# Optimization experiments

Hardware: AMD Instinct MI355X
Metric: run time of the kernel (lower is better)

The kernel has to match this reference:

```python
import jax, jax.numpy as jnp
import numpy as np

EMBED = 256
NHEAD = 8
HDIM = EMBED // NHEAD
EPS = 1e-6


def setup_inputs() -> dict:
    key = jax.random.key(0)
    ks = jax.random.split(key, 10)
    B, L, E = 8, 8192, EMBED
    sc = 1.0 / np.sqrt(E)
    return {
        "q": jax.random.normal(ks[0], (B, L, E), jnp.float32),
        "k": jax.random.normal(ks[1], (B, L, E), jnp.float32),
        "v": jax.random.normal(ks[2], (B, L, E), jnp.float32),
        "Wq": jax.random.normal(ks[3], (E, E), jnp.float32) * sc,
        "bq": jax.random.normal(ks[4], (E,), jnp.float32) * 0.01,
        "Wk": jax.random.normal(ks[5], (E, E), jnp.float32) * sc,
        "bk": jax.random.normal(ks[6], (E,), jnp.float32) * 0.01,
        "Wv": jax.random.normal(ks[7], (E, E), jnp.float32) * sc,
        "bv": jax.random.normal(ks[8], (E,), jnp.float32) * 0.01,
        "Wm": jax.random.normal(ks[9], (E, E), jnp.float32) * sc,
    }


def _feature_map(x):
    # elu(x) + 1, the LoFTR linear-attention kernel feature map
    return jax.nn.elu(x) + 1.0


def reference(q, k, v, Wq, bq, Wk, bk, Wv, bv, Wm):
    B, L, E = q.shape
    # QKV projections (nn.Linear: x @ W.T + b), split into heads
    Q = (q @ Wq.T + bq).reshape(B, L, NHEAD, HDIM)
    K = (k @ Wk.T + bk).reshape(B, -1, NHEAD, HDIM)
    V = (v @ Wv.T + bv).reshape(B, -1, NHEAD, HDIM)

    Qf = _feature_map(Q)              # [B,L,H,D]
    Kf = _feature_map(K)              # [B,S,H,D]
    v_len = V.shape[1]
    Vn = V / v_len
    # KV: per-head outer-product accumulation over source positions
    KV = jnp.einsum("bshd,bshv->bhdv", Kf, Vn)       # [B,H,D,D]
    Ksum = Kf.sum(axis=1)                              # [B,H,D]
    Z = 1.0 / (jnp.einsum("blhd,bhd->blh", Qf, Ksum) + EPS)  # [B,L,H]
    msg = jnp.einsum("blhd,bhdv,blh->blhv", Qf, KV, Z) * v_len  # [B,L,H,D]
    # merge heads and output projection (bias=False)
    out = msg.reshape(B, L, NHEAD * HDIM) @ Wm.T
    return out
```

## Files before the change

kernel.cpp:

```cpp
#include <hip/hip_runtime.h>
#include <hip/hip_bf16.h>

#define SEQ   8192
#define NB    8
#define EMB   256
#define NHD   8
#define HDM   32
#define LDP   72

typedef __attribute__((ext_vector_type(8))) short short8;
typedef __attribute__((ext_vector_type(4))) float floatx4;
typedef __attribute__((ext_vector_type(16))) float floatx16;

__device__ __forceinline__ short f2b(float f) {
    __hip_bfloat16 h = __float2bfloat16(f);
    return __builtin_bit_cast(short, h);
}
__device__ __forceinline__ float b2f(short s) {
    unsigned u = (unsigned)(unsigned short)s << 16;
    return __builtin_bit_cast(float, u);
}

__device__ __forceinline__ void gload16(const void* g, void* l) {
    __builtin_amdgcn_global_load_lds(
        (const __attribute__((address_space(1))) unsigned*)g,
        (__attribute__((address_space(3))) unsigned*)l, 16, 0, 0);
}

__launch_bounds__(256)
__global__ void wconv_kernel(const float* __restrict__ Wq,
                             const float* __restrict__ Wk,
                             const float* __restrict__ Wv,
                             short* __restrict__ Wb) {
    const float* src = (blockIdx.y == 0) ? Wq : (blockIdx.y == 1) ? Wk : Wv;
    const int i = (blockIdx.x * 256 + threadIdx.x) * 8;
    float4 f0 = *(const float4*)(src + i);
    float4 f1 = *(const float4*)(src + i + 4);
    short8 o;
    o[0] = f2b(f0.x); o[1] = f2b(f0.y); o[2] = f2b(f0.z); o[3] = f2b(f0.w);
    o[4] = f2b(f1.x); o[5] = f2b(f1.y); o[6] = f2b(f1.z); o[7] = f2b(f1.w);
    *(short8*)(Wb + (size_t)blockIdx.y * 65536 + i) = o;
}

__launch_bounds__(256)
__global__ void qkv_kernel(const float* __restrict__ qin,
                           const float* __restrict__ kin,
                           const float* __restrict__ vin,
                           const short* __restrict__ Wb,
                           const float* __restrict__ bq,
                           const float* __restrict__ bk,
                           const float* __restrict__ bv,
                           short* __restrict__ Qf, short* __restrict__ Kf,
                           short* __restrict__ Vn,
                           float* __restrict__ Ksum) {
    __shared__ __align__(16) float As[128 * 64];
    __shared__ __align__(16) short Bs[128 * 64];
    __shared__ float colsum[128];

    const int tid  = threadIdx.x;
    const int tm   = blockIdx.x;
    const int tn   = blockIdx.y;
    const int mode = blockIdx.z;
    const int lane = tid & 63;
    const int wave = tid >> 6;
    const int wm   = (wave & 1) << 6;
    const int wn   = (wave >> 1) << 6;
    const int fr   = lane & 15;
    const int fq   = lane >> 4;

    const float* X    = (mode == 0) ? qin : (mode == 1) ? kin : vin;
    const float* bias = (mode == 0) ? bq  : (mode == 1) ? bk  : bv;
    short*       out  = (mode == 0) ? Qf  : (mode == 1) ? Kf  : Vn;

    if (mode == 1 && tid < 128) colsum[tid] = 0.f;

    const float* Xb = X + (size_t)(tm * 128) * EMB;
    const short* Wt = Wb + (size_t)mode * 65536 + (size_t)(tn * 128) * EMB;

    floatx4 acc[4][4];
    #pragma unroll
    for (int i = 0; i < 4; i++)
        #pragma unroll
        for (int j = 0; j < 4; j++)
            #pragma unroll
            for (int r = 0; r < 4; r++) acc[i][j][r] = 0.f;

    for (int kc = 0; kc < 4; kc++) {
        const int kb = kc * 64;
        #pragma unroll
        for (int u = 0; u < 8; u++) {
            const int c   = u * 256 + tid;
            const int row = c >> 4;
            const int q   = c & 15;
            const int col = (((q >> 1) ^ (row & 7)) << 3) + ((q & 1) << 2);
            gload16(Xb + (size_t)row * EMB + kb + col, &As[c * 4]);
        }
        #pragma unroll
        for (int u = 0; u < 4; u++) {
            const int c   = u * 256 + tid;
            const int row = c >> 3;
            const int q   = c & 7;
            const int col = ((q ^ (row & 7)) << 3);
            gload16(Wt + (size_t)row * EMB + kb + col, &Bs[c * 8]);
        }
        __syncthreads();
        #pragma unroll
        for (int kk = 0; kk < 64; kk += 32) {
            short8 a[4], b[4];
            #pragma unroll
            for (int i = 0; i < 4; i++) {
                const int row  = wm + i * 16 + fr;
                const int P    = (kk >> 3) + fq;
                const int base = row * 64 + (((P ^ (row & 7)) << 3));
                float4 x0 = *(const float4*)&As[base];
                float4 x1 = *(const float4*)&As[base + 4];
                short8 t;
                t[0] = f2b(x0.x); t[1] = f2b(x0.y); t[2] = f2b(x0.z); t[3] = f2b(x0.w);
                t[4] = f2b(x1.x); t[5] = f2b(x1.y); t[6] = f2b(x1.z); t[7] = f2b(x1.w);
                a[i] = t;
            }
            #pragma unroll
            for (int j = 0; j < 4; j++) {
                const int row = wn + j * 16 + fr;
                const int qB  = (kk >> 3) + fq;
                b[j] = *(const short8*)&Bs[row * 64 + ((qB ^ (row & 7)) << 3)];
            }
            #pragma unroll
            for (int i = 0; i < 4; i++)
                #pragma unroll
                for (int j = 0; j < 4; j++)
                    acc[i][j] = __builtin_amdgcn_mfma_f32_16x16x32_bf16(a[i], b[j], acc[i][j], 0, 0, 0);
        }
        __syncthreads();
    }

    const int row0 = tm * 128;
    float ks[4] = {0.f, 0.f, 0.f, 0.f};
    #pragma unroll
    for (int i = 0; i < 4; i++) {
        #pragma unroll
        for (int j = 0; j < 4; j++) {
            const int colg = tn * 128 + wn + j * 16 + fr;
            const float bia = bias[colg];
            #pragma unroll
            for (int rr = 0; rr < 4; rr++) {
                const int rowg = row0 + wm + i * 16 + fq * 4 + rr;
                float v = acc[i][j][rr] + bia;
                if (mode <= 1) v = (v > 0.f) ? (v + 1.f) : __expf(v);
                else           v *= (1.0f / (float)SEQ);
                out[(size_t)rowg * EMB + colg] = f2b(v);
                ks[j] += v;
            }
        }
    }
    if (mode == 1) {
        #pragma unroll
        for (int j = 0; j < 4; j++)
            atomicAdd(&colsum[wn + j * 16 + fr], ks[j]);
        __syncthreads();
        if (tid < 128) {
            const int b = (tm * 128) / SEQ;
            atomicAdd(&Ksum[b * EMB + tn * 128 + tid], colsum[tid]);
        }
    }
}

template <bool ATOMIC>
__launch_bounds__(256)
__global__ void kv_kernel(const short* __restrict__ Kf,
                          const short* __restrict__ Vn,
                          float* __restrict__ dst_base,
                          int kvsp) {
    __shared__ __align__(16) short Kt[32 * 256];
    __shared__ __align__(16) short Vt[32 * 256];

    const int tid  = threadIdx.x;
    const int sp   = blockIdx.x % kvsp;
    const int b    = blockIdx.x / kvsp;
    const int wave = tid >> 6;
    const int lane = tid & 63;
    const int h    = wave * 2 + (lane >> 5);
    const int l5   = lane & 31;
    const int d0   = (l5 >> 2) * 4;
    const int v0   = (l5 & 3) * 8;
    const int chunk = SEQ / kvsp;
    const size_t rowbase = (size_t)(b * SEQ + sp * chunk) * EMB;

    float acc[4][8];
    #pragma unroll
    for (int i = 0; i < 4; i++)
        #pragma unroll
        for (int j = 0; j < 8; j++) acc[i][j] = 0.f;

    for (int t0 = 0; t0 < chunk; t0 += 32) {
        __syncthreads();
        const short* ksrc = Kf + rowbase + (size_t)t0 * EMB;
        const short* vsrc = Vn + rowbase + (size_t)t0 * EMB;
        #pragma unroll
        for (int u = 0; u < 4; u++) {
            const int c   = tid + u * 256;
            const int row = c >> 5;
            const int col = (c & 31) * 8;
            *(short8*)&Kt[row * 256 + col] = *(const short8*)(ksrc + (size_t)row * EMB + col);
            *(short8*)&Vt[row * 256 + col] = *(const short8*)(vsrc + (size_t)row * EMB + col);
        }
        __syncthreads();
        #pragma unroll 4
        for (int s = 0; s < 32; s++) {
            short4 k4 = *(const short4*)&Kt[s * 256 + h * 32 + d0];
            short8 v8 = *(const short8*)&Vt[s * 256 + h * 32 + v0];
            float kf[4] = {b2f(k4.x), b2f(k4.y), b2f(k4.z), b2f(k4.w)};
            float vf[8];
            #pragma unroll
            for (int j = 0; j < 8; j++) vf[j] = b2f(v8[j]);
            #pragma unroll
            for (int i = 0; i < 4; i++)
                #pragma unroll
                for (int j = 0; j < 8; j++) acc[i][j] += kf[i] * vf[j];
        }
    }

    if (ATOMIC) {
        float* dst = dst_base + (size_t)((b * 8 + h) * 1024);
        #pragma unroll
        for (int i = 0; i < 4; i++)
            #pragma unroll
            for (int j = 0; j < 8; j++)
                atomicAdd(&dst[(d0 + i) * 32 + v0 + j], acc[i][j]);
    } else {
        float* dst = dst_base + (size_t)(((size_t)sp * NB + b) * 8 + h) * 1024;
        #pragma unroll
        for (int i = 0; i < 4; i++) {
            float4 lo = make_float4(acc[i][0], acc[i][1], acc[i][2], acc[i][3]);
            float4 hi = make_float4(acc[i][4], acc[i][5], acc[i][6], acc[i][7]);
            *(float4*)&dst[(d0 + i) * 32 + v0]     = lo;
            *(float4*)&dst[(d0 + i) * 32 + v0 + 4] = hi;
        }
    }
}

__launch_bounds__(256)
__global__ void kvred_kernel(const float* __restrict__ KVp,
                             float* __restrict__ KV, int kvsp) {
    const int i = blockIdx.x * 1024 + threadIdx.x * 4;
    float4 s = make_float4(0.f, 0.f, 0.f, 0.f);
    for (int p = 0; p < kvsp; p++) {
        float4 t = *(const float4*)&KVp[(size_t)p * 65536 + i];
        s.x += t.x; s.y += t.y; s.z += t.z; s.w += t.w;
    }
    *(float4*)&KV[i] = s;
}

__launch_bounds__(64)
__global__ void m_kernel(const float* __restrict__ KV,
                         const float* __restrict__ Wm,
                         short* __restrict__ Mt) {
    const int blk  = blockIdx.x;
    const int e0   = (blk & 7) * 32;
    const int h    = (blk >> 3) & 7;
    const int b    = blk >> 6;
    const int lane = threadIdx.x;
    const int l31  = lane & 31;
    const int q    = lane >> 5;

    floatx16 acc;
    #pragma unroll
    for (int i = 0; i < 16; i++) acc[i] = 0.f;

    #pragma unroll
    for (int kb = 0; kb < 32; kb += 16) {
        const float* ar = KV + (size_t)(((b * 8 + h) * 32 + l31) * 32) + kb + q * 8;
        const float* br = Wm + (size_t)(e0 + l31) * EMB + h * 32 + kb + q * 8;
        short8 a, w;
        #pragma unroll
        for (int t = 0; t < 8; t++) { a[t] = f2b(ar[t]); w[t] = f2b(br[t]); }
        acc = __builtin_amdgcn_mfma_f32_32x32x16_bf16(a, w, acc, 0, 0, 0);
    }

    short* mrow = Mt + (size_t)b * EMB * EMB + (size_t)(e0 + l31) * EMB + h * 32;
    #pragma unroll
    for (int r4 = 0; r4 < 4; r4++) {
        const int dbase = 8 * r4 + 4 * q;
        short4 s4 = make_short4(f2b(acc[r4 * 4 + 0]), f2b(acc[r4 * 4 + 1]),
                                f2b(acc[r4 * 4 + 2]), f2b(acc[r4 * 4 + 3]));
        *(short4*)(mrow + dbase) = s4;
    }
}

__launch_bounds__(256)
__global__ void out_kernel(const short* __restrict__ Qf,
                           const float* __restrict__ Ksum,
                           const short* __restrict__ Mt,
                           float* __restrict__ Out) {
    __shared__ __align__(16) short As[128 * LDP];
    __shared__ __align__(16) short Bs[128 * LDP];
    __shared__ float zs[128][NHD];
    __shared__ float ksl[EMB];

    const int tid  = threadIdx.x;
    const int tm   = blockIdx.x;
    const int tn   = blockIdx.y;
    const int b    = (tm * 128) / SEQ;
    const int lane = tid & 63;
    const int wave = tid >> 6;
    const int wm   = (wave & 1) << 6;
    const int wn   = (wave >> 1) << 6;
    const int fr   = lane & 15;
    const int fq   = lane >> 4;

    ksl[tid] = Ksum[b * EMB + tid];
    __syncthreads();

    {
        const int t  = tid >> 1;
        const int h0 = (tid & 1) * 4;
        const short* qrow = Qf + (size_t)(tm * 128 + t) * EMB;
        #pragma unroll
        for (int hh = 0; hh < 4; hh++) {
            const int h = h0 + hh;
            float d = 0.f;
            #pragma unroll
            for (int u = 0; u < 8; u++) {
                short4 q4 = *(const short4*)(qrow + h * 32 + 4 * u);
                d += b2f(q4.x) * ksl[h * 32 + 4 * u + 0] + b2f(q4.y) * ksl[h * 32 + 4 * u + 1]
                   + b2f(q4.z) * ksl[h * 32 + 4 * u + 2] + b2f(q4.w) * ksl[h * 32 + 4 * u + 3];
            }
            zs[t][h] = (float)SEQ / (d + 1e-6f);
        }
    }
    __syncthreads();

    floatx4 acc[4][4];
    #pragma unroll
    for (int i = 0; i < 4; i++)
        #pragma unroll
        for (int j = 0; j < 4; j++)
            #pragma unroll
            for (int r = 0; r < 4; r++) acc[i][j][r] = 0.f;

    const short* Ab = Qf + (size_t)(tm * 128) * EMB;
    const short* Bb = Mt + (size_t)b * EMB * EMB + (size_t)(tn * 128) * EMB;

    for (int kc = 0; kc < 4; kc++) {
        const int kb = kc * 64;
        #pragma unroll
        for (int u = 0; u < 4; u++) {
            const int g   = u * 256 + tid;
            const int row = g >> 3;
            const int c8  = (g & 7) * 8;
            const float z = zs[row][(kb + c8) >> 5];
            short8 qv = *(const short8*)(Ab + (size_t)row * EMB + kb + c8);
            short8 oa;
            #pragma unroll
            for (int t = 0; t < 8; t++) oa[t] = f2b(b2f(qv[t]) * z);
            *(short8*)&As[row * LDP + c8] = oa;
            *(short8*)&Bs[row * LDP + c8] = *(const short8*)(Bb + (size_t)row * EMB + kb + c8);
        }
        __syncthreads();
        #pragma unroll
        for (int kk = 0; kk < 64; kk += 32) {
            short8 a[4], bb[4];
            #pragma unroll
            for (int i = 0; i < 4; i++)
                a[i] = *(const short8*)&As[(wm + i * 16 + fr) * LDP + kk + fq * 8];
            #pragma unroll
            for (int j = 0; j < 4; j++)
                bb[j] = *(const short8*)&Bs[(wn + j * 16 + fr) * LDP + kk + fq * 8];
            #pragma unroll
            for (int i = 0; i < 4; i++)
                #pragma unroll
                for (int j = 0; j < 4; j++)
                    acc[i][j] = __builtin_amdgcn_mfma_f32_16x16x32_bf16(a[i], bb[j], acc[i][j], 0, 0, 0);
        }
        __syncthreads();
    }

    const int row0 = tm * 128;
    #pragma unroll
    for (int i = 0; i < 4; i++) {
        #pragma unroll
        for (int j = 0; j < 4; j++) {
            const int colg = tn * 128 + wn + j * 16 + fr;
            #pragma unroll
            for (int rr = 0; rr < 4; rr++) {
                const int rowg = row0 + wm + i * 16 + fq * 4 + rr;
                Out[(size_t)rowg * EMB + colg] = acc[i][j][rr];
            }
        }
    }
}

extern "C" void kernel_launch(void* const* d_in, const int* in_sizes, int n_in,
                              void* d_out, int out_size, void* d_ws, size_t ws_size,
                              hipStream_t stream) {
    (void)in_sizes; (void)n_in; (void)out_size;
    const float* q  = (const float*)d_in[0];
    const float* k  = (const float*)d_in[1];
    const float* v  = (const float*)d_in[2];
    const float* Wq = (const float*)d_in[3];
    const float* bq = (const float*)d_in[4];
    const float* Wk = (const float*)d_in[5];
    const float* bk = (const float*)d_in[6];
    const float* Wv = (const float*)d_in[7];
    const float* bv = (const float*)d_in[8];
    const float* Wm = (const float*)d_in[9];

    char* ws = (char*)d_ws;
    short* Qf   = (short*)(ws);
    short* Kf   = (short*)(ws + 33554432);
    short* Vn   = (short*)(ws + 67108864);
    float* Ksum = (float*)(ws + 100663296);
    float* KV   = (float*)(ws + 100663296 + 8192);
    short* Mt   = (short*)(ws + 100663296 + 8192 + 262144);
    short* Wb   = (short*)(ws + 100663296 + 8192 + 262144);
    const size_t kvp_off = 100663296ull + 8192 + 262144 + 1048576;
    float* KVp  = (float*)(ws + kvp_off);

    int kvsp = 0;
    if      (ws_size >= kvp_off + 64ull * 262144) kvsp = 64;
    else if (ws_size >= kvp_off + 32ull * 262144) kvsp = 32;
    else if (ws_size >= kvp_off + 16ull * 262144) kvsp = 16;

    hipMemsetAsync(ws + 100663296, 0, 8192 + 262144, stream);

    dim3 blk(256);
    wconv_kernel<<<dim3(32, 3), blk, 0, stream>>>(Wq, Wk, Wv, Wb);
    qkv_kernel<<<dim3(512, 2, 3), blk, 0, stream>>>(q, k, v, Wb, bq, bk, bv,
                                                    Qf, Kf, Vn, Ksum);

    if (kvsp) {
        kv_kernel<false><<<NB * kvsp, 256, 0, stream>>>(Kf, Vn, KVp, kvsp);
        kvred_kernel<<<64, 256, 0, stream>>>(KVp, KV, kvsp);
    } else {
        kv_kernel<true><<<NB * 16, 256, 0, stream>>>(Kf, Vn, KV, 16);
    }

    m_kernel<<<512, 64, 0, stream>>>(KV, Wm, Mt);
    out_kernel<<<dim3(512, 2), blk, 0, stream>>>(Qf, Ksum, Mt, (float*)d_out);
}
```

Measured before the change: 388.9 us.

## Register-prefetch next K-chunk across qkv, kv, and out kernels with lightweight barriers

Replaces the direct global-to-LDS async loads in the QKV projection with register-staged prefetching. The next chunk's global loads are issued before the barrier so they overlap the current chunk's MFMA work, and the same double-buffering-through-registers scheme is applied to the KV accumulation and output kernels. The QKV kernel now converts X to bf16 once when writing LDS, stored in a padded bf16 layout, instead of storing fp32 in a swizzled layout and converting at every fragment read. It also adds a custom barrier that waits only on LDS counters, and occupancy hints via launch_bounds. The costs are higher register pressure and the loss of the direct-to-LDS load path.

```diff
diff --git a/kernel.cpp b/kernel.cpp
--- a/kernel.cpp
+++ b/kernel.cpp
@@ -21,10 +21,11 @@
     return __builtin_bit_cast(float, u);
 }
 
-__device__ __forceinline__ void gload16(const void* g, void* l) {
-    __builtin_amdgcn_global_load_lds(
-        (const __attribute__((address_space(1))) unsigned*)g,
-        (__attribute__((address_space(3))) unsigned*)l, 16, 0, 0);
+__device__ __forceinline__ void lds_barrier() {
+    asm volatile("s_waitcnt lgkmcnt(0)" ::: "memory");
+    __builtin_amdgcn_sched_barrier(0);
+    __builtin_amdgcn_s_barrier();
+    __builtin_amdgcn_sched_barrier(0);
 }
 
 __launch_bounds__(256)
@@ -42,7 +43,7 @@
     *(short8*)(Wb + (size_t)blockIdx.y * 65536 + i) = o;
 }
 
-__launch_bounds__(256)
+__launch_bounds__(256, 3)
 __global__ void qkv_kernel(const float* __restrict__ qin,
                            const float* __restrict__ kin,
                            const float* __restrict__ vin,
@@ -53,8 +54,8 @@
                            short* __restrict__ Qf, short* __restrict__ Kf,
                            short* __restrict__ Vn,
                            float* __restrict__ Ksum) {
-    __shared__ __align__(16) float As[128 * 64];
-    __shared__ __align__(16) short Bs[128 * 64];
+    __shared__ __align__(16) short As[128 * LDP];
+    __shared__ __align__(16) short Bs[128 * LDP];
     __shared__ float colsum[128];
 
     const int tid  = threadIdx.x;
@@ -85,53 +86,60 @@
             #pragma unroll
             for (int r = 0; r < 4; r++) acc[i][j][r] = 0.f;
 
+    float4 pa[8];
+    short8 pw[4];
+
+    auto loadA = [&](int kc) {
+        const int kb = kc * 64;
+        #pragma unroll
+        for (int u = 0; u < 8; u++) {
+            const int g = u * 256 + tid;
+            pa[u] = *(const float4*)(Xb + (size_t)(g >> 4) * EMB + kb + (g & 15) * 4);
+        }
+    };
+    auto loadW = [&](int kc) {
+        const int kb = kc * 64;
+        #pragma unroll
+        for (int u = 0; u < 4; u++) {
+            const int g = u * 256 + tid;
+            pw[u] = *(const short8*)(Wt + (size_t)(g >> 3) * EMB + kb + (g & 7) * 8);
+        }
+    };
+
+    loadA(0); loadW(0);
+
     for (int kc = 0; kc < 4; kc++) {
-        const int kb = kc * 64;
         #pragma unroll
         for (int u = 0; u < 8; u++) {
-            const int c   = u * 256 + tid;
-            const int row = c >> 4;
-            const int q   = c & 15;
-            const int col = (((q >> 1) ^ (row & 7)) << 3) + ((q & 1) << 2);
-            gload16(Xb + (size_t)row * EMB + kb + col, &As[c * 4]);
-        }
-        #pragma unroll
-        for (int u = 0; u < 4; u++) {
-            const int c   = u * 256 + tid;
-            const int row = c >> 3;
-            const int q   = c & 7;
-            const int col = ((q ^ (row & 7)) << 3);
-            gload16(Wt + (size_t)row * EMB + kb + col, &Bs[c * 8]);
-        }
-        __syncthreads();
+            const int g = u * 256 + tid;
+            const int row = g >> 4, c4 = (g & 15) * 4;
+            *(short4*)&As[row * LDP + c4] =
+                make_short4(f2b(pa[u].x), f2b(pa[u].y), f2b(pa[u].z), f2b(pa[u].w));
+        }
+        #pragma unroll
+        for (int u = 0; u < 4; u++) {
+            const int g = u * 256 + tid;
+            *(short8*)&Bs[(g >> 3) * LDP + (g & 7) * 8] = pw[u];
+        }
+        if (kc < 3) { loadA(kc + 1); loadW(kc + 1); }
+        lds_barrier();
+
         #pragma unroll
         for (int kk = 0; kk < 64; kk += 32) {
             short8 a[4], b[4];
             #pragma unroll
-            for (int i = 0; i < 4; i++) {
-                const int row  = wm + i * 16 + fr;
-                const int P    = (kk >> 3) + fq;
-                const int base = row * 64 + (((P ^ (row & 7)) << 3));
-                float4 x0 = *(const float4*)&As[base];
-                float4 x1 = *(const float4*)&As[base + 4];
-                short8 t;
-                t[0] = f2b(x0.x); t[1] = f2b(x0.y); t[2] = f2b(x0.z); t[3] = f2b(x0.w);
-                t[4] = f2b(x1.x); t[5] = f2b(x1.y); t[6] = f2b(x1.z); t[7] = f2b(x1.w);
-                a[i] = t;
-            }
-            #pragma unroll
-            for (int j = 0; j < 4; j++) {
-                const int row = wn + j * 16 + fr;
-                const int qB  = (kk >> 3) + fq;
-                b[j] = *(const short8*)&Bs[row * 64 + ((qB ^ (row & 7)) << 3)];
-            }
+            for (int i = 0; i < 4; i++)
+                a[i] = *(const short8*)&As[(wm + i * 16 + fr) * LDP + kk + fq * 8];
+            #pragma unroll
+            for (int j = 0; j < 4; j++)
+                b[j] = *(const short8*)&Bs[(wn + j * 16 + fr) * LDP + kk + fq * 8];
             #pragma unroll
             for (int i = 0; i < 4; i++)
                 #pragma unroll
                 for (int j = 0; j < 4; j++)
                     acc[i][j] = __builtin_amdgcn_mfma_f32_16x16x32_bf16(a[i], b[j], acc[i][j], 0, 0, 0);
         }
-        __syncthreads();
+        lds_barrier();
     }
 
     const int row0 = tm * 128;
@@ -192,8 +200,8 @@
         #pragma unroll
         for (int j = 0; j < 8; j++) acc[i][j] = 0.f;
 
-    for (int t0 = 0; t0 < chunk; t0 += 32) {
-        __syncthreads();
+    short8 pk[4], pv[4];
+    auto loadKV = [&](int t0) {
         const short* ksrc = Kf + rowbase + (size_t)t0 * EMB;
         const short* vsrc = Vn + rowbase + (size_t)t0 * EMB;
         #pragma unroll
@@ -201,10 +209,23 @@
             const int c   = tid + u * 256;
             const int row = c >> 5;
             const int col = (c & 31) * 8;
-            *(short8*)&Kt[row * 256 + col] = *(const short8*)(ksrc + (size_t)row * EMB + col);
-            *(short8*)&Vt[row * 256 + col] = *(const short8*)(vsrc + (size_t)row * EMB + col);
-        }
-        __syncthreads();
+            pk[u] = *(const short8*)(ksrc + (size_t)row * EMB + col);
+            pv[u] = *(const short8*)(vsrc + (size_t)row * EMB + col);
+        }
+    };
+
+    loadKV(0);
+    for (int t0 = 0; t0 < chunk; t0 += 32) {
+        #pragma unroll
+        for (int u = 0; u < 4; u++) {
+            const int c   = tid + u * 256;
+            const int row = c >> 5;
+            const int col = (c & 31) * 8;
+            *(short8*)&Kt[row * 256 + col] = pk[u];
+            *(short8*)&Vt[row * 256 + col] = pv[u];
+        }
+        if (t0 + 32 < chunk) loadKV(t0 + 32);
+        lds_barrier();
         #pragma unroll 4
         for (int s = 0; s < 32; s++) {
             short4 k4 = *(const short4*)&Kt[s * 256 + h * 32 + d0];
@@ -218,6 +239,7 @@
                 #pragma unroll
                 for (int j = 0; j < 8; j++) acc[i][j] += kf[i] * vf[j];
         }
+        lds_barrier();
     }
 
     if (ATOMIC) {
@@ -287,7 +309,7 @@
     }
 }
 
-__launch_bounds__(256)
+__launch_bounds__(256, 3)
 __global__ void out_kernel(const short* __restrict__ Qf,
                            const float* __restrict__ Ksum,
                            const short* __restrict__ Mt,
@@ -341,22 +363,34 @@
     const short* Ab = Qf + (size_t)(tm * 128) * EMB;
     const short* Bb = Mt + (size_t)b * EMB * EMB + (size_t)(tn * 128) * EMB;
 
+    short8 pq[4], pm[4];
+    auto loadQM = [&](int kc) {
+        const int kb = kc * 64;
+        #pragma unroll
+        for (int u = 0; u < 4; u++) {
+            const int g = u * 256 + tid;
+            const int row = g >> 3, c8 = (g & 7) * 8;
+            pq[u] = *(const short8*)(Ab + (size_t)row * EMB + kb + c8);
+            pm[u] = *(const short8*)(Bb + (size_t)row * EMB + kb + c8);
+        }
+    };
+
+    loadQM(0);
     for (int kc = 0; kc < 4; kc++) {
         const int kb = kc * 64;
         #pragma unroll
         for (int u = 0; u < 4; u++) {
-            const int g   = u * 256 + tid;
-            const int row = g >> 3;
-            const int c8  = (g & 7) * 8;
+            const int g = u * 256 + tid;
+            const int row = g >> 3, c8 = (g & 7) * 8;
             const float z = zs[row][(kb + c8) >> 5];
-            short8 qv = *(const short8*)(Ab + (size_t)row * EMB + kb + c8);
             short8 oa;
             #pragma unroll
-            for (int t = 0; t < 8; t++) oa[t] = f2b(b2f(qv[t]) * z);
+            for (int t = 0; t < 8; t++) oa[t] = f2b(b2f(pq[u][t]) * z);
             *(short8*)&As[row * LDP + c8] = oa;
-            *(short8*)&Bs[row * LDP + c8] = *(const short8*)(Bb + (size_t)row * EMB + kb + c8);
-        }
-        __syncthreads();
+            *(short8*)&Bs[row * LDP + c8] = pm[u];
+        }
+        if (kc < 3) loadQM(kc + 1);
+        lds_barrier();
         #pragma unroll
         for (int kk = 0; kk < 64; kk += 32) {
             short8 a[4], bb[4];
@@ -372,7 +406,7 @@
                 for (int j = 0; j < 4; j++)
                     acc[i][j] = __builtin_amdgcn_mfma_f32_16x16x32_bf16(a[i], bb[j], acc[i][j], 0, 0, 0);
         }
-        __syncthreads();
+        lds_barrier();
     }
 
     const int row0 = tm * 128;
```

Result: no change. 385.6 us (-0.8%).
